# Performance work log

Measured on AMD Instinct MI355X. Metric: run time of the kernel, lower is better.

## Reference

```python
import jax, jax.numpy as jnp
import numpy as np

B, T, V, E, H, C = 256, 512, 100000, 128, 256, 2


def setup_inputs() -> dict:
    key = jax.random.key(0)
    ks = jax.random.split(key, 14)
    lens = jax.random.randint(ks[0], (B,), 1, T + 1)          # valid lengths in [1, T]
    seqs = jax.random.randint(ks[1], (B, T), 1, V)            # tokens 1..V-1 (0 = pad)
    valid = jnp.arange(T)[None, :] < lens[:, None]
    seqs = jnp.where(valid, seqs, 0)                           # padding_idx = 0
    embed = jax.random.normal(ks[2], (V, E), dtype=jnp.float32) * 0.02
    embed = embed.at[0].set(0.0)                               # padding row zeroed (torch padding_idx)
    s = 1.0 / np.sqrt(H)
    u = lambda k, sh: jax.random.uniform(k, sh, minval=-s, maxval=s, dtype=jnp.float32)
    return {
        "seqs": seqs, "lens": lens, "embed": embed,
        "W_ih_f": u(ks[3], (3 * H, E)), "W_hh_f": u(ks[4], (3 * H, H)),
        "b_ih_f": u(ks[5], (3 * H,)),   "b_hh_f": u(ks[6], (3 * H,)),
        "W_ih_b": u(ks[7], (3 * H, E)), "W_hh_b": u(ks[8], (3 * H, H)),
        "b_ih_b": u(ks[9], (3 * H,)),   "b_hh_b": u(ks[10], (3 * H,)),
        "W_fc": u(ks[11], (C, 2 * H)),  "b_fc": u(ks[12], (C,)),
    }


def _gru_last_hidden(x, W_ih, W_hh, b_ih, b_hh, lens):
    """Run a single-direction GRU over x [B,T,E]; return hidden at step lens-1, [B,H].
    PyTorch GRU gate order: r, z, n."""
    xp = jnp.einsum('bte,ge->btg', x, W_ih) + b_ih             # [B,T,3H], one big GEMM up front

    def step(h, xp_t):                                          # xp_t: [B,3H]
        hp = h @ W_hh.T + b_hh
        r = jax.nn.sigmoid(xp_t[:, :H] + hp[:, :H])
        z = jax.nn.sigmoid(xp_t[:, H:2 * H] + hp[:, H:2 * H])
        n = jnp.tanh(xp_t[:, 2 * H:] + r * hp[:, 2 * H:])
        h_new = (1.0 - z) * n + z * h
        return h_new, h_new

    h0 = jnp.zeros((x.shape[0], H), dtype=x.dtype)
    _, hs = jax.lax.scan(step, h0, jnp.swapaxes(xp, 0, 1))     # hs: [T,B,H]
    return hs[lens - 1, jnp.arange(x.shape[0])]                # hidden at last valid step


def reference(seqs, lens, embed, W_ih_f, W_hh_f, b_ih_f, b_hh_f,
              W_ih_b, W_hh_b, b_ih_b, b_hh_b, W_fc, b_fc):
    x = embed[seqs]                                            # [B,T,E]
    # forward direction: final hidden at t = len-1 (packed-sequence semantics)
    h_f = _gru_last_hidden(x, W_ih_f, W_hh_f, b_ih_f, b_hh_f, lens)
    # backward direction: reverse each sequence within its valid length, then same scan
    idx = jnp.clip(lens[:, None] - 1 - jnp.arange(T)[None, :], 0, T - 1)  # [B,T]
    x_rev = jnp.take_along_axis(x, idx[:, :, None], axis=1)
    h_b = _gru_last_hidden(x_rev, W_ih_b, W_hh_b, b_ih_b, b_hh_b, lens)
    h = jnp.concatenate([h_f, h_b], axis=1)                    # [B,2H]
    return h @ W_fc.T + b_fc                                   # [B,C]
```

## Files before the change

### kernel.cpp

```cpp
#include <hip/hip_runtime.h>
#include <cstdint>
#include <cstddef>

#define B_   256
#define T_   512
#define E_   128
#define H_   256

typedef _Float16 f16x8 __attribute__((ext_vector_type(8)));
typedef _Float16 f16x4 __attribute__((ext_vector_type(4)));
typedef float    f32x4 __attribute__((ext_vector_type(4)));

__device__ __forceinline__ float sigm(float x) {
  return __builtin_amdgcn_rcpf(1.f + __expf(-x));
}
__device__ __forceinline__ float tanh_(float x) {
  float e = __expf(2.f * x);
  return 1.f - 2.f * __builtin_amdgcn_rcpf(1.f + e);
}
__device__ __forceinline__ void poll_ge(const int* p, int v) {
  while (__hip_atomic_load(p, __ATOMIC_ACQUIRE, __HIP_MEMORY_SCOPE_AGENT) < v)
    __builtin_amdgcn_s_sleep(4);
}

__global__ __launch_bounds__(256) void prep_kernel(
    const float* __restrict__ whhf, const float* __restrict__ whhb,
    const float* __restrict__ wihf, const float* __restrict__ wihb,
    _Float16* __restrict__ WSW,
    const int* __restrict__ lens, int* __restrict__ order, int* __restrict__ flags)
{
  if (blockIdx.x == 288) {
    int i = threadIdx.x;
    for (int k = i; k < 1024; k += 256) flags[k] = 0;
    for (int k = i; k < 512;  k += 256) flags[1024 + k] = -1;
    int li = lens[i];
    int rank = 0;
    for (int k = 0; k < B_; ++k) {
      int lk = lens[k];
      rank += (lk > li) || (lk == li && k < i);
    }
    order[rank] = i;
    return;
  }
  int idx = blockIdx.x * 256 + threadIdx.x;
  int lane = idx & 63;
  int tile = (idx >> 6) % 48;
  int kc   = (idx / 3072) % 12;
  int dir  = idx / 36864;
  int ncol = tile * 16 + (lane & 15);
  int quad = lane >> 4;
  const float* src;
  if (kc < 8) {
    const float* w = dir ? whhb : whhf;
    src = w + (size_t)ncol * H_ + kc * 32 + quad * 8;
  } else {
    const float* w = dir ? wihb : wihf;
    src = w + (size_t)ncol * E_ + (kc - 8) * 32 + quad * 8;
  }
  f16x8 v;
  #pragma unroll
  for (int j = 0; j < 8; ++j) v[j] = (_Float16)src[j];
  *(f16x8*)(WSW + (size_t)idx * 8) = v;
}

#define XPSLAB 196608
__global__ __launch_bounds__(512, 1) void fused_kernel(
    const _Float16* __restrict__ WSW, const int* __restrict__ seqs,
    const float* __restrict__ embed,
    const float* __restrict__ bihf, const float* __restrict__ bhhf,
    const float* __restrict__ bihb, const float* __restrict__ bhhb,
    const int* __restrict__ lens, const int* __restrict__ order,
    _Float16* __restrict__ XP, int* __restrict__ FLAGS, float* __restrict__ hcat)
{
  __shared__ __align__(16) char smem[17408];
  __shared__ int s_row[16], s_len[16];

  const int bid = blockIdx.x, tid = threadIdx.x;
  const int w = tid >> 6, lane = tid & 63, lm = lane & 15, lq = lane >> 4;

  if (bid < 32) {
    const int g = bid, dir = g & 1, grp = g >> 1;
    _Float16* hb = (_Float16*)smem;
    if (tid < 16) { int r = order[grp * 16 + tid]; s_row[tid] = r; s_len[tid] = lens[r]; }
    for (int i = tid; i < 2 * 16 * 264; i += 512) hb[i] = (_Float16)0.f;

    const _Float16* wsd = WSW + (size_t)dir * 294912 + (size_t)lane * 8;
    f16x8 wh[6][8];
    #pragma unroll
    for (int kc = 0; kc < 8; ++kc) {
      wh[0][kc] = *(const f16x8*)(wsd + (size_t)kc * 24576 + (2 * w)      * 512);
      wh[1][kc] = *(const f16x8*)(wsd + (size_t)kc * 24576 + (2 * w + 1)  * 512);
      wh[2][kc] = *(const f16x8*)(wsd + (size_t)kc * 24576 + (16 + 2 * w) * 512);
      wh[3][kc] = *(const f16x8*)(wsd + (size_t)kc * 24576 + (17 + 2 * w) * 512);
      wh[4][kc] = *(const f16x8*)(wsd + (size_t)kc * 24576 + (32 + 2 * w) * 512);
      wh[5][kc] = *(const f16x8*)(wsd + (size_t)kc * 24576 + (33 + 2 * w) * 512);
    }
    const float* bhh = dir ? bhhb : bhhf;
    f16x4 bhn[2];
    #pragma unroll
    for (int th = 0; th < 2; ++th) {
      float4 b = *(const float4*)(bhh + 512 + 32 * w + th * 16 + lq * 4);
      bhn[th][0] = (_Float16)b.x; bhn[th][1] = (_Float16)b.y;
      bhn[th][2] = (_Float16)b.z; bhn[th][3] = (_Float16)b.w;
    }
    __syncthreads();
    const int len_l = s_len[lm];
    int ml = 1;
    #pragma unroll
    for (int i = 0; i < 16; ++i) ml = max(ml, s_len[i]);

    int* doneP  = FLAGS + 1024 + g * 16;
    const int* readyA = FLAGS + g * 32;
    const int* readyB = FLAGS + g * 32 + 16;
    float h32r[2][4] = {};

    for (int t = 0; t < ml; ++t) {
      if ((t & 15) == 0) {
        if (tid == 0) {
          if (t) __hip_atomic_store(doneP, (t >> 4) - 1,
                                    __ATOMIC_RELEASE, __HIP_MEMORY_SCOPE_AGENT);
          poll_ge(readyA, (t >> 4) + 1);
          poll_ge(readyB, (t >> 4) + 1);
        }
        __syncthreads();
      }
      const _Float16* sb = XP + ((size_t)((((t >> 4) & 1) * 32 + g)) * 16 + (t & 15)) * 12288
                           + lq * 64 + lm * 4;
      f16x4 xp[6];
      xp[0] = *(const f16x4*)(sb + (2 * w)      * 256);
      xp[1] = *(const f16x4*)(sb + (2 * w + 1)  * 256);
      xp[2] = *(const f16x4*)(sb + (16 + 2 * w) * 256);
      xp[3] = *(const f16x4*)(sb + (17 + 2 * w) * 256);
      xp[4] = *(const f16x4*)(sb + (32 + 2 * w) * 256);
      xp[5] = *(const f16x4*)(sb + (33 + 2 * w) * 256);

      f32x4 acc[6] = {};
      const _Float16* hrow = hb + ((size_t)(t & 1) * 16 + lm) * 264 + lq * 8;
      #pragma unroll
      for (int kc = 0; kc < 8; ++kc) {
        f16x8 hf = *(const f16x8*)(hrow + kc * 32);
        acc[0] = __builtin_amdgcn_mfma_f32_16x16x32_f16(wh[0][kc], hf, acc[0], 0, 0, 0);
        acc[1] = __builtin_amdgcn_mfma_f32_16x16x32_f16(wh[1][kc], hf, acc[1], 0, 0, 0);
        acc[2] = __builtin_amdgcn_mfma_f32_16x16x32_f16(wh[2][kc], hf, acc[2], 0, 0, 0);
        acc[3] = __builtin_amdgcn_mfma_f32_16x16x32_f16(wh[3][kc], hf, acc[3], 0, 0, 0);
        acc[4] = __builtin_amdgcn_mfma_f32_16x16x32_f16(wh[4][kc], hf, acc[4], 0, 0, 0);
        acc[5] = __builtin_amdgcn_mfma_f32_16x16x32_f16(wh[5][kc], hf, acc[5], 0, 0, 0);
      }
      #pragma unroll
      for (int th = 0; th < 2; ++th) {
        f16x4 pk;
        #pragma unroll
        for (int i = 0; i < 4; ++i) {
          float r = sigm((float)xp[th][i]     + acc[th][i]);
          float z = sigm((float)xp[2 + th][i] + acc[2 + th][i]);
          float n = tanh_((float)xp[4 + th][i] + r * (acc[4 + th][i] + (float)bhn[th][i]));
          float hn = (t < len_l) ? (n + z * (h32r[th][i] - n)) : h32r[th][i];
          h32r[th][i] = hn;
          pk[i] = (_Float16)hn;
        }
        *(f16x4*)(hb + ((size_t)((t + 1) & 1) * 16 + lm) * 264 + 32 * w + th * 16 + lq * 4) = pk;
      }
      __syncthreads();
    }
    if (tid == 0)
      __hip_atomic_store(doneP, 999, __ATOMIC_RELEASE, __HIP_MEMORY_SCOPE_AGENT);
    {
      const int rowb = s_row[lm];
      #pragma unroll
      for (int th = 0; th < 2; ++th) {
        float4 o; o.x = h32r[th][0]; o.y = h32r[th][1]; o.z = h32r[th][2]; o.w = h32r[th][3];
        *(float4*)(&hcat[(size_t)rowb * (2 * H_) + dir * H_ + 32 * w + th * 16 + lq * 4]) = o;
      }
    }
  } else {
    const int k_ = bid - 32;
    const int g = (k_ & 7) + 8 * (k_ >> 4), half = (k_ >> 3) & 1;
    const int dir = g & 1, grp = g >> 1;
    _Float16* xs = (_Float16*)smem;
    if (tid < 16) { int r = order[grp * 16 + tid]; s_row[tid] = r; s_len[tid] = lens[r]; }
    __syncthreads();
    int ml = 1;
    #pragma unroll
    for (int i = 0; i < 16; ++i) ml = max(ml, s_len[i]);
    const int nch = (ml + 15) >> 4;

    const int chain = tid >> 5, q = tid & 31;
    const int rowb = s_row[chain], lenr = s_len[chain];
    const _Float16* wsd = WSW + (size_t)dir * 294912 + (size_t)lane * 8;
    const float* bih = dir ? bihb : bihf;
    const float* bhh = dir ? bhhb : bhhf;
    const int* doneP = FLAGS + 1024 + g * 16;
    int* readyP = FLAGS + g * 32 + half * 16;

    f16x8 wA[6][4];
    float bb[6][4];
    #pragma unroll
    for (int ti = 0; ti < 6; ++ti) {
      const int tile = w + 8 * ti;
      #pragma unroll
      for (int kc = 0; kc < 4; ++kc)
        wA[ti][kc] = *(const f16x8*)(wsd + (size_t)(8 + kc) * 24576 + tile * 512);
      float4 bias = *(const float4*)(bih + tile * 16 + lq * 4);
      if (tile < 32) {
        float4 b2 = *(const float4*)(bhh + tile * 16 + lq * 4);
        bias.x += b2.x; bias.y += b2.y; bias.z += b2.z; bias.w += b2.w;
      }
      bb[ti][0] = bias.x; bb[ti][1] = bias.y; bb[ti][2] = bias.z; bb[ti][3] = bias.w;
    }

    for (int c = 0; c < nch; ++c) {
      if (c >= 2) { if (tid == 0) poll_ge(doneP, c - 2); __syncthreads(); }
      _Float16* slab = XP + (size_t)((c & 1) * 32 + g) * XPSLAB;
      #pragma unroll
      for (int batch = 0; batch < 2; ++batch) {
        #pragma unroll
        for (int sb = 0; sb < 4; ++sb) {
          int s = c * 16 + half * 8 + batch * 4 + sb;
          int p = dir ? (lenr - 1 - s) : s;
          p = min(max(p, 0), T_ - 1);
          int tok = seqs[(size_t)rowb * T_ + p];
          float4 f = *(const float4*)(embed + (size_t)tok * E_ + q * 4);
          f16x4 h4; h4[0] = (_Float16)f.x; h4[1] = (_Float16)f.y;
          h4[2] = (_Float16)f.z; h4[3] = (_Float16)f.w;
          *(f16x4*)(xs + ((size_t)sb * 16 + chain) * 136 + q * 4) = h4;
        }
        __syncthreads();
        f16x8 bx[4][4];
        #pragma unroll
        for (int sb = 0; sb < 4; ++sb)
          #pragma unroll
          for (int kc = 0; kc < 4; ++kc)
            bx[sb][kc] = *(const f16x8*)(xs + ((size_t)sb * 16 + lm) * 136 + kc * 32 + lq * 8);
        #pragma unroll
        for (int ti = 0; ti < 6; ++ti) {
          const int tile = w + 8 * ti;
          f32x4 acc[4] = {};
          #pragma unroll
          for (int kc = 0; kc < 4; ++kc) {
            acc[0] = __builtin_amdgcn_mfma_f32_16x16x32_f16(wA[ti][kc], bx[0][kc], acc[0], 0, 0, 0);
            acc[1] = __builtin_amdgcn_mfma_f32_16x16x32_f16(wA[ti][kc], bx[1][kc], acc[1], 0, 0, 0);
            acc[2] = __builtin_amdgcn_mfma_f32_16x16x32_f16(wA[ti][kc], bx[2][kc], acc[2], 0, 0, 0);
            acc[3] = __builtin_amdgcn_mfma_f32_16x16x32_f16(wA[ti][kc], bx[3][kc], acc[3], 0, 0, 0);
          }
          #pragma unroll
          for (int sb = 0; sb < 4; ++sb) {
            int s_local = half * 8 + batch * 4 + sb;
            f16x4 o;
            #pragma unroll
            for (int i = 0; i < 4; ++i) o[i] = (_Float16)(acc[sb][i] + bb[ti][i]);
            *(f16x4*)(slab + (size_t)s_local * 12288 + tile * 256 + lq * 64 + lm * 4) = o;
          }
        }
        __syncthreads();
      }
      if (tid == 0)
        __hip_atomic_store(readyP, c + 1, __ATOMIC_RELEASE, __HIP_MEMORY_SCOPE_AGENT);
    }
  }
}

__global__ __launch_bounds__(512) void fc_kernel(
    const float* __restrict__ hcat, const float* __restrict__ wfc,
    const float* __restrict__ bfc, float* __restrict__ out)
{
  const int b = blockIdx.x, t = threadIdx.x;
  float h  = hcat[(size_t)b * 512 + t];
  float p0 = h * wfc[t];
  float p1 = h * wfc[512 + t];
  #pragma unroll
  for (int off = 32; off > 0; off >>= 1) {
    p0 += __shfl_down(p0, off);
    p1 += __shfl_down(p1, off);
  }
  __shared__ float s0[8], s1[8];
  if ((t & 63) == 0) { s0[t >> 6] = p0; s1[t >> 6] = p1; }
  __syncthreads();
  if (t == 0) {
    float a = bfc[0], c = bfc[1];
    #pragma unroll
    for (int i = 0; i < 8; ++i) { a += s0[i]; c += s1[i]; }
    out[b * 2 + 0] = a;
    out[b * 2 + 1] = c;
  }
}

extern "C" void kernel_launch(void* const* d_in, const int* in_sizes, int n_in,
                              void* d_out, int out_size, void* d_ws, size_t ws_size,
                              hipStream_t stream)
{
  (void)in_sizes; (void)n_in; (void)out_size; (void)ws_size;
  const int*   seqs  = (const int*)d_in[0];
  const int*   lens  = (const int*)d_in[1];
  const float* embed = (const float*)d_in[2];
  const float* wihf  = (const float*)d_in[3];
  const float* whhf  = (const float*)d_in[4];
  const float* bihf  = (const float*)d_in[5];
  const float* bhhf  = (const float*)d_in[6];
  const float* wihb  = (const float*)d_in[7];
  const float* whhb  = (const float*)d_in[8];
  const float* bihb  = (const float*)d_in[9];
  const float* bhhb  = (const float*)d_in[10];
  const float* wfc   = (const float*)d_in[11];
  const float* bfc   = (const float*)d_in[12];
  float* out = (float*)d_out;

  char* ws = (char*)d_ws;
  _Float16* WSW = (_Float16*)ws;
  size_t off = 1179648;
  _Float16* XP  = (_Float16*)(ws + off); off += (size_t)2 * 32 * XPSLAB * 2;
  float* HCAT   = (float*)(ws + off);    off += (size_t)B_ * 2 * H_ * 4;
  int* ORDER    = (int*)(ws + off);      off += 1024;
  int* FLAGS    = (int*)(ws + off);      off += 6144;

  prep_kernel<<<289, 256, 0, stream>>>(whhf, whhb, wihf, wihb, WSW, lens, ORDER, FLAGS);
  fused_kernel<<<96, 512, 0, stream>>>(WSW, seqs, embed, bihf, bhhf, bihb, bhhb,
                                       lens, ORDER, XP, FLAGS, HCAT);
  fc_kernel<<<B_, 512, 0, stream>>>(HCAT, wfc, bfc, out);
}
```

Before: 1.268 ms.

## Split each GRU recurrence group across two blocks exchanging hidden halves

Each recurrent group (16 sequences, one direction) is now handled by two workgroups, each owning half of the hidden units. At every timestep the two blocks exchange their half of h through a global buffer, synchronised with per-step atomic counters. This halves the per-step MFMA and gate work per block and doubles the number of CUs on the serial recurrence. The cost is a cross-CU flag poll and a global memory round trip on every one of the up to 512 steps, plus a grid that grows from 96 to 128 blocks, all of which must be co-resident for the spin-waits to make progress.

Result: slower. 3.190 ms (+151.5%).

```diff
diff --git a/kernel.cpp b/kernel.cpp
--- a/kernel.cpp
+++ b/kernel.cpp
@@ -32,7 +32,7 @@
   if (blockIdx.x == 288) {
     int i = threadIdx.x;
     for (int k = i; k < 1024; k += 256) flags[k] = 0;
-    for (int k = i; k < 512;  k += 256) flags[1024 + k] = -1;
+    for (int k = i; k < 640;  k += 256) flags[1024 + k] = -1;
     int li = lens[i];
     int rank = 0;
     for (int k = 0; k < B_; ++k) {
@@ -70,7 +70,8 @@
     const float* __restrict__ bihf, const float* __restrict__ bhhf,
     const float* __restrict__ bihb, const float* __restrict__ bhhb,
     const int* __restrict__ lens, const int* __restrict__ order,
-    _Float16* __restrict__ XP, int* __restrict__ FLAGS, float* __restrict__ hcat)
+    _Float16* __restrict__ XP, _Float16* __restrict__ HX,
+    int* __restrict__ FLAGS, float* __restrict__ hcat)
 {
   __shared__ __align__(16) char smem[17408];
   __shared__ int s_row[16], s_len[16];
@@ -78,102 +79,124 @@
   const int bid = blockIdx.x, tid = threadIdx.x;
   const int w = tid >> 6, lane = tid & 63, lm = lane & 15, lq = lane >> 4;
 
-  if (bid < 32) {
-    const int g = bid, dir = g & 1, grp = g >> 1;
+  if (bid < 64) {
+    const int g = bid & 31, hf = bid >> 5, po = 1 - hf;
+    const int dir = g & 1, grp = g >> 1;
     _Float16* hb = (_Float16*)smem;
     if (tid < 16) { int r = order[grp * 16 + tid]; s_row[tid] = r; s_len[tid] = lens[r]; }
-    for (int i = tid; i < 2 * 16 * 264; i += 512) hb[i] = (_Float16)0.f;
-
+    for (int i = tid; i < 2 * 16 * 136; i += 512) hb[i] = (_Float16)0.f;
+    {
+      f16x4 z4 = {};
+      *(f16x4*)(HX + ((size_t)(g * 2 + hf) * 2 + 0) * 2048 + tid * 4) = z4;
+    }
     const _Float16* wsd = WSW + (size_t)dir * 294912 + (size_t)lane * 8;
-    f16x8 wh[6][8];
+    f16x8 whr[8], whz[8], whn[8];
     #pragma unroll
     for (int kc = 0; kc < 8; ++kc) {
-      wh[0][kc] = *(const f16x8*)(wsd + (size_t)kc * 24576 + (2 * w)      * 512);
-      wh[1][kc] = *(const f16x8*)(wsd + (size_t)kc * 24576 + (2 * w + 1)  * 512);
-      wh[2][kc] = *(const f16x8*)(wsd + (size_t)kc * 24576 + (16 + 2 * w) * 512);
-      wh[3][kc] = *(const f16x8*)(wsd + (size_t)kc * 24576 + (17 + 2 * w) * 512);
-      wh[4][kc] = *(const f16x8*)(wsd + (size_t)kc * 24576 + (32 + 2 * w) * 512);
-      wh[5][kc] = *(const f16x8*)(wsd + (size_t)kc * 24576 + (33 + 2 * w) * 512);
+      whr[kc] = *(const f16x8*)(wsd + (size_t)kc * 24576 + (hf * 8 + w)      * 512);
+      asm volatile("" : "+a"(whr[kc]));
+      whz[kc] = *(const f16x8*)(wsd + (size_t)kc * 24576 + (16 + hf * 8 + w) * 512);
+      asm volatile("" : "+a"(whz[kc]));
+      whn[kc] = *(const f16x8*)(wsd + (size_t)kc * 24576 + (32 + hf * 8 + w) * 512);
+      asm volatile("" : "+a"(whn[kc]));
     }
     const float* bhh = dir ? bhhb : bhhf;
-    f16x4 bhn[2];
-    #pragma unroll
-    for (int th = 0; th < 2; ++th) {
-      float4 b = *(const float4*)(bhh + 512 + 32 * w + th * 16 + lq * 4);
-      bhn[th][0] = (_Float16)b.x; bhn[th][1] = (_Float16)b.y;
-      bhn[th][2] = (_Float16)b.z; bhn[th][3] = (_Float16)b.w;
+    f16x4 bhn;
+    {
+      float4 b = *(const float4*)(bhh + 512 + hf * 128 + w * 16 + lq * 4);
+      bhn[0] = (_Float16)b.x; bhn[1] = (_Float16)b.y;
+      bhn[2] = (_Float16)b.z; bhn[3] = (_Float16)b.w;
     }
     __syncthreads();
+    int* mineC = FLAGS + 1536 + g * 2 + hf;
+    const int* peerC = FLAGS + 1536 + g * 2 + po;
+    if (tid == 0)
+      __hip_atomic_store(mineC, 0, __ATOMIC_RELEASE, __HIP_MEMORY_SCOPE_AGENT);
+
     const int len_l = s_len[lm];
     int ml = 1;
     #pragma unroll
     for (int i = 0; i < 16; ++i) ml = max(ml, s_len[i]);
 
-    int* doneP  = FLAGS + 1024 + g * 16;
+    int* doneP  = FLAGS + 1024 + g * 16 + hf * 8;
     const int* readyA = FLAGS + g * 32;
     const int* readyB = FLAGS + g * 32 + 16;
-    float h32r[2][4] = {};
+    float h32r[4] = {};
 
     for (int t = 0; t < ml; ++t) {
-      if ((t & 15) == 0) {
-        if (tid == 0) {
+      if (tid == 0) {
+        if ((t & 15) == 0) {
           if (t) __hip_atomic_store(doneP, (t >> 4) - 1,
                                     __ATOMIC_RELEASE, __HIP_MEMORY_SCOPE_AGENT);
           poll_ge(readyA, (t >> 4) + 1);
           poll_ge(readyB, (t >> 4) + 1);
         }
-        __syncthreads();
-      }
+        poll_ge(peerC, t);
+      }
+      __syncthreads();
+      const _Float16* hp = HX + ((size_t)(g * 2 + po) * 2 + (t & 1)) * 2048
+                           + lm * 128 + lq * 8;
+      f16x8 hp0 = *(const f16x8*)(hp);
+      f16x8 hp1 = *(const f16x8*)(hp + 32);
+      f16x8 hp2 = *(const f16x8*)(hp + 64);
+      f16x8 hp3 = *(const f16x8*)(hp + 96);
       const _Float16* sb = XP + ((size_t)((((t >> 4) & 1) * 32 + g)) * 16 + (t & 15)) * 12288
                            + lq * 64 + lm * 4;
-      f16x4 xp[6];
-      xp[0] = *(const f16x4*)(sb + (2 * w)      * 256);
-      xp[1] = *(const f16x4*)(sb + (2 * w + 1)  * 256);
-      xp[2] = *(const f16x4*)(sb + (16 + 2 * w) * 256);
-      xp[3] = *(const f16x4*)(sb + (17 + 2 * w) * 256);
-      xp[4] = *(const f16x4*)(sb + (32 + 2 * w) * 256);
-      xp[5] = *(const f16x4*)(sb + (33 + 2 * w) * 256);
-
-      f32x4 acc[6] = {};
-      const _Float16* hrow = hb + ((size_t)(t & 1) * 16 + lm) * 264 + lq * 8;
-      #pragma unroll
-      for (int kc = 0; kc < 8; ++kc) {
-        f16x8 hf = *(const f16x8*)(hrow + kc * 32);
-        acc[0] = __builtin_amdgcn_mfma_f32_16x16x32_f16(wh[0][kc], hf, acc[0], 0, 0, 0);
-        acc[1] = __builtin_amdgcn_mfma_f32_16x16x32_f16(wh[1][kc], hf, acc[1], 0, 0, 0);
-        acc[2] = __builtin_amdgcn_mfma_f32_16x16x32_f16(wh[2][kc], hf, acc[2], 0, 0, 0);
-        acc[3] = __builtin_amdgcn_mfma_f32_16x16x32_f16(wh[3][kc], hf, acc[3], 0, 0, 0);
-        acc[4] = __builtin_amdgcn_mfma_f32_16x16x32_f16(wh[4][kc], hf, acc[4], 0, 0, 0);
-        acc[5] = __builtin_amdgcn_mfma_f32_16x16x32_f16(wh[5][kc], hf, acc[5], 0, 0, 0);
-      }
-      #pragma unroll
-      for (int th = 0; th < 2; ++th) {
-        f16x4 pk;
-        #pragma unroll
-        for (int i = 0; i < 4; ++i) {
-          float r = sigm((float)xp[th][i]     + acc[th][i]);
-          float z = sigm((float)xp[2 + th][i] + acc[2 + th][i]);
-          float n = tanh_((float)xp[4 + th][i] + r * (acc[4 + th][i] + (float)bhn[th][i]));
-          float hn = (t < len_l) ? (n + z * (h32r[th][i] - n)) : h32r[th][i];
-          h32r[th][i] = hn;
-          pk[i] = (_Float16)hn;
-        }
-        *(f16x4*)(hb + ((size_t)((t + 1) & 1) * 16 + lm) * 264 + 32 * w + th * 16 + lq * 4) = pk;
-      }
+      f16x4 xr = *(const f16x4*)(sb + (hf * 8 + w)      * 256);
+      f16x4 xz = *(const f16x4*)(sb + (16 + hf * 8 + w) * 256);
+      f16x4 xn = *(const f16x4*)(sb + (32 + hf * 8 + w) * 256);
+
+      f32x4 ar = {}, az = {}, an;
+      #pragma unroll
+      for (int i = 0; i < 4; ++i) an[i] = (float)bhn[i];
+
+      const _Float16* hrow = hb + ((size_t)(t & 1) * 16 + lm) * 136 + lq * 8;
+      #pragma unroll
+      for (int kco = 0; kco < 4; ++kco) {
+        f16x8 hfr = *(const f16x8*)(hrow + kco * 32);
+        ar = __builtin_amdgcn_mfma_f32_16x16x32_f16(whr[hf * 4 + kco], hfr, ar, 0, 0, 0);
+        az = __builtin_amdgcn_mfma_f32_16x16x32_f16(whz[hf * 4 + kco], hfr, az, 0, 0, 0);
+        an = __builtin_amdgcn_mfma_f32_16x16x32_f16(whn[hf * 4 + kco], hfr, an, 0, 0, 0);
+      }
+      ar = __builtin_amdgcn_mfma_f32_16x16x32_f16(whr[po * 4 + 0], hp0, ar, 0, 0, 0);
+      az = __builtin_amdgcn_mfma_f32_16x16x32_f16(whz[po * 4 + 0], hp0, az, 0, 0, 0);
+      an = __builtin_amdgcn_mfma_f32_16x16x32_f16(whn[po * 4 + 0], hp0, an, 0, 0, 0);
+      ar = __builtin_amdgcn_mfma_f32_16x16x32_f16(whr[po * 4 + 1], hp1, ar, 0, 0, 0);
+      az = __builtin_amdgcn_mfma_f32_16x16x32_f16(whz[po * 4 + 1], hp1, az, 0, 0, 0);
+      an = __builtin_amdgcn_mfma_f32_16x16x32_f16(whn[po * 4 + 1], hp1, an, 0, 0, 0);
+      ar = __builtin_amdgcn_mfma_f32_16x16x32_f16(whr[po * 4 + 2], hp2, ar, 0, 0, 0);
+      az = __builtin_amdgcn_mfma_f32_16x16x32_f16(whz[po * 4 + 2], hp2, az, 0, 0, 0);
+      an = __builtin_amdgcn_mfma_f32_16x16x32_f16(whn[po * 4 + 2], hp2, an, 0, 0, 0);
+      ar = __builtin_amdgcn_mfma_f32_16x16x32_f16(whr[po * 4 + 3], hp3, ar, 0, 0, 0);
+      az = __builtin_amdgcn_mfma_f32_16x16x32_f16(whz[po * 4 + 3], hp3, az, 0, 0, 0);
+      an = __builtin_amdgcn_mfma_f32_16x16x32_f16(whn[po * 4 + 3], hp3, an, 0, 0, 0);
+
+      f16x4 pk;
+      #pragma unroll
+      for (int i = 0; i < 4; ++i) {
+        float r = sigm((float)xr[i] + ar[i]);
+        float z = sigm((float)xz[i] + az[i]);
+        float n = tanh_((float)xn[i] + r * an[i]);
+        float hn = (t < len_l) ? (n + z * (h32r[i] - n)) : h32r[i];
+        h32r[i] = hn;
+        pk[i] = (_Float16)hn;
+      }
+      *(f16x4*)(hb + ((size_t)((t + 1) & 1) * 16 + lm) * 136 + w * 16 + lq * 4) = pk;
+      *(f16x4*)(HX + ((size_t)(g * 2 + hf) * 2 + ((t + 1) & 1)) * 2048
+                + lm * 128 + w * 16 + lq * 4) = pk;
       __syncthreads();
+      if (tid == 0)
+        __hip_atomic_store(mineC, t + 1, __ATOMIC_RELEASE, __HIP_MEMORY_SCOPE_AGENT);
     }
     if (tid == 0)
       __hip_atomic_store(doneP, 999, __ATOMIC_RELEASE, __HIP_MEMORY_SCOPE_AGENT);
     {
       const int rowb = s_row[lm];
-      #pragma unroll
-      for (int th = 0; th < 2; ++th) {
-        float4 o; o.x = h32r[th][0]; o.y = h32r[th][1]; o.z = h32r[th][2]; o.w = h32r[th][3];
-        *(float4*)(&hcat[(size_t)rowb * (2 * H_) + dir * H_ + 32 * w + th * 16 + lq * 4]) = o;
-      }
+      float4 o; o.x = h32r[0]; o.y = h32r[1]; o.z = h32r[2]; o.w = h32r[3];
+      *(float4*)(&hcat[(size_t)rowb * (2 * H_) + dir * H_ + hf * 128 + w * 16 + lq * 4]) = o;
     }
   } else {
-    const int k_ = bid - 32;
+    const int k_ = bid - 64;
     const int g = (k_ & 7) + 8 * (k_ >> 4), half = (k_ >> 3) & 1;
     const int dir = g & 1, grp = g >> 1;
     _Float16* xs = (_Float16*)smem;
@@ -189,7 +212,8 @@
     const _Float16* wsd = WSW + (size_t)dir * 294912 + (size_t)lane * 8;
     const float* bih = dir ? bihb : bihf;
     const float* bhh = dir ? bhhb : bhhf;
-    const int* doneP = FLAGS + 1024 + g * 16;
+    const int* doneA = FLAGS + 1024 + g * 16;
+    const int* doneB = FLAGS + 1024 + g * 16 + 8;
     int* readyP = FLAGS + g * 32 + half * 16;
 
     f16x8 wA[6][4];
@@ -209,7 +233,10 @@
     }
 
     for (int c = 0; c < nch; ++c) {
-      if (c >= 2) { if (tid == 0) poll_ge(doneP, c - 2); __syncthreads(); }
+      if (c >= 2) {
+        if (tid == 0) { poll_ge(doneA, c - 2); poll_ge(doneB, c - 2); }
+        __syncthreads();
+      }
       _Float16* slab = XP + (size_t)((c & 1) * 32 + g) * XPSLAB;
       #pragma unroll
       for (int batch = 0; batch < 2; ++batch) {
@@ -310,10 +337,11 @@
   _Float16* XP  = (_Float16*)(ws + off); off += (size_t)2 * 32 * XPSLAB * 2;
   float* HCAT   = (float*)(ws + off);    off += (size_t)B_ * 2 * H_ * 4;
   int* ORDER    = (int*)(ws + off);      off += 1024;
-  int* FLAGS    = (int*)(ws + off);      off += 6144;
+  int* FLAGS    = (int*)(ws + off);      off += 8192;
+  _Float16* HX  = (_Float16*)(ws + off); off += (size_t)32 * 2 * 2 * 2048 * 2;
 
   prep_kernel<<<289, 256, 0, stream>>>(whhf, whhb, wihf, wihb, WSW, lens, ORDER, FLAGS);
-  fused_kernel<<<96, 512, 0, stream>>>(WSW, seqs, embed, bihf, bhhf, bihb, bhhb,
-                                       lens, ORDER, XP, FLAGS, HCAT);
+  fused_kernel<<<128, 512, 0, stream>>>(WSW, seqs, embed, bihf, bhhf, bihb, bhhb,
+                                        lens, ORDER, XP, HX, FLAGS, HCAT);
   fc_kernel<<<B_, 512, 0, stream>>>(HCAT, wfc, bfc, out);
 }
```
